# Optimization experiments

Hardware: AMD Instinct MI355X
Metric: run time of the kernel (lower is better)

## Reference

```python
import jax, jax.numpy as jnp
import numpy as np

SMOOTH = 1e-3
EPS = 1e-12


def setup_inputs() -> dict:
    key = jax.random.key(0)
    k1, k2, k3 = jax.random.split(key, 3)
    pred = jax.random.normal(k1, (1, 16, 384, 384), dtype=jnp.float32)
    labels = jax.random.randint(k2, (1, 16, 384, 384), 0, 2, dtype=jnp.int32)
    # stand-in for create_table_neighbour_code_to_surface_area((1,1,1)): 256-entry LUT
    area = jax.random.uniform(k3, (256,), dtype=jnp.float32) * 2.0
    return {"pred": pred, "labels": labels, "area": area}


def _corners(x2):
    # x2: (B, 2, Y+2, X+2) zero-padded slice pair -> (B, 8, (Y+1)*(X+1))
    # corner index k = dz*4 + dy*2 + dx, matching torch unfold(kernel=(2,2), padding=1)
    B, _, Yp, Xp = x2.shape
    Y, X = Yp - 1, Xp - 1
    cs = [x2[:, dz, dy:dy + Y, dx:dx + X]
          for dz in (0, 1) for dy in (0, 1) for dx in (0, 1)]
    return jnp.stack(cs, axis=1).reshape(B, 8, Y * X)


def _surface_dice(pred_sig, labels, area, smooth):
    B, Z, Y, X = pred_sig.shape
    # bases[i, k] = bit k of code i  (== [c=='1' for c in f'{i:08b}'[::-1]])
    bits = jnp.arange(8, dtype=jnp.int32)
    bases = ((jnp.arange(256, dtype=jnp.int32)[:, None] >> bits[None, :]) & 1).astype(jnp.float32)  # (256,8)
    n_bits = bases.sum(1)  # (256,) popcount

    # blank zero slices on both z ends + the unfold's zero padding in y/x
    Pp = jnp.pad(pred_sig, ((0, 0), (1, 1), (1, 1), (1, 1)))
    Lp = jnp.pad(labels.astype(jnp.int32), ((0, 0), (1, 1), (1, 1), (1, 1)))

    def pair(carry, i):
        num, den, vol = carry
        pz = jax.lax.dynamic_slice(Pp, (0, i, 0, 0), (B, 2, Y + 2, X + 2))
        lz = jax.lax.dynamic_slice(Lp, (0, i, 0, 0), (B, 2, Y + 2, X + 2))
        pc = _corners(pz)                      # (B, 8, Np) float
        lc = _corners(lz)                      # (B, 8, Np) int32
        byte = jnp.left_shift(lc, bits[None, :, None]).sum(axis=1)  # (B, Np) label corner code

        # basis_weights = 1 - mean_k (pc_k - bases_ik)^2, expanded so the
        # (B,256,8,Np) broadcast is never materialized
        sp2 = jnp.sum(pc * pc, axis=1)                       # (B, Np)
        cross = jnp.einsum('bkn,ik->bin', pc, bases)         # (B, 256, Np)
        bw = 1.0 - (sp2[:, None, :] + n_bits[None, :, None] - 2.0 * cross) / 8.0

        pred_byte = jnp.argmax(bw, axis=1)                   # (B, Np)
        pred_area = area[pred_byte]                          # (B, Np)
        label_area = area[byte]                              # (B, Np)
        pw = jnp.take_along_axis(bw, byte[:, None, :], axis=1)[:, 0]  # (B, Np)

        # binary_cross_entropy(unfolded_pred, unfolded_labels) per element
        lf = lc.astype(jnp.float32)
        logp = jnp.log(jnp.maximum(pc, EPS))
        log1mp = jnp.log(jnp.maximum(1.0 - pc, EPS))
        bce = -(lf * logp + (1.0 - lf) * log1mp)             # (B, 8, Np)
        interior = (byte == 0) | (byte == 255)               # (B, Np)
        v = jnp.where(interior[:, None, :], bce, 0.0).mean((1, 2))

        inter = jnp.sum(pw * label_area, axis=1)
        return (num + 2.0 * inter,
                den + label_area.sum(1) + pred_area.sum(1),
                vol + v), None

    init = (jnp.zeros((B,), jnp.float32), jnp.zeros((B,), jnp.float32), jnp.zeros((B,), jnp.float32))
    (num, den, vol), _ = jax.lax.scan(pair, init, jnp.arange(Z + 1))
    dice = 1.0 - (num + smooth) / (den + smooth)
    return dice.mean() + vol.mean()


def reference(pred, labels, area):
    return _surface_dice(jax.nn.sigmoid(pred), labels, area, SMOOTH)
```

## Files before the change

kernel.cpp:

```cpp
#include <hip/hip_runtime.h>
#include <math.h>

constexpr int ZN = 16, YN = 384, XN = 384;
constexpr int NZ = 17, NY = 385, NX = 385;
constexpr int NP = NY * NX;
constexpr int NROWS = NZ * NY;
constexpr int BLOCKS = 1637;

__global__ __launch_bounds__(256) void sd_main(
        const float* __restrict__ pred,
        const int*   __restrict__ labels,
        const float* __restrict__ area,
        float*       __restrict__ partial)
{
    __shared__ float s_area[256];
    {
        const int t = threadIdx.x;
        const int own = t >> 4, prv = t & 15;
        int code = 0;
#pragma unroll
        for (int r = 0; r < 4; ++r)
            code |= (((prv >> r) & 1) << (2 * r)) | (((own >> r) & 1) << (2 * r + 1));
        s_area[t] = area[code];
    }
    __syncthreads();

    const int lane = threadIdx.x & 63;
    const int wid  = blockIdx.x * 4 + (threadIdx.x >> 6);

    float num = 0.f, den = 0.f, vol = 0.f;

    if (wid < NROWS) {
        const int z = wid / NY;
        const int y = wid - z * NY;

        bool rv[4]; int base[4];
#pragma unroll
        for (int r = 0; r < 4; ++r) {
            const int zz = z - 1 + (r >> 1);
            const int yy = y - 1 + (r & 1);
            rv[r]   = ((unsigned)zz < (unsigned)ZN) & ((unsigned)yy < (unsigned)YN);
            base[r] = (zz * YN + yy) * XN;
        }

        float cs[4] = {0.f, 0.f, 0.f, 0.f};
        int   cb = 0;

        auto do_node = [&](const float s[4], int LP, const float ps[4], int PLP) {
            const int idxL = ((LP & 15) << 4) | (PLP & 15);
            const int idxP = (LP & 0xF0) | (PLP >> 4);
            const float la = s_area[idxL];
            const float pa = s_area[idxP];
            float u[8];
            float sq = 0.f;
#pragma unroll
            for (int r = 0; r < 4; ++r) {
                const float u0 = ((PLP >> r) & 1) ? ps[r] : 1.f - ps[r];
                const float u1 = ((LP  >> r) & 1) ? s[r]  : 1.f - s[r];
                u[2 * r] = u0; u[2 * r + 1] = u1;
                const float d0 = 1.f - u0, d1 = 1.f - u1;
                sq += d0 * d0 + d1 * d1;
            }
            const float pw = 1.f - sq * 0.125f;
            num += 2.f * pw * la;
            den += la + pa;
            if (idxL == 0 || idxL == 255) {
                float b = 0.f;
#pragma unroll
                for (int k = 0; k < 8; ++k)
                    b += __logf(fmaxf(u[k], 1e-12f));
                vol -= b;
            }
        };

        for (int chunk = 0; chunk < 6; ++chunk) {
            const int x = chunk * 64 + lane;
            float s[4]; int LP = 0;
#pragma unroll
            for (int r = 0; r < 4; ++r) {
                if (rv[r]) {
                    const float p = pred[base[r] + x];
                    const int   l = labels[base[r] + x];
                    s[r] = __fdividef(1.f, 1.f + __expf(-p));
                    LP  |= (l << r) | ((int)(p > 0.f) << (r + 4));
                } else {
                    s[r] = 0.f;
                }
            }
            float ps[4]; int PLP;
#pragma unroll
            for (int r = 0; r < 4; ++r) ps[r] = __shfl_up(s[r], 1);
            PLP = __shfl_up(LP, 1);
            if (lane == 0) {
#pragma unroll
                for (int r = 0; r < 4; ++r) ps[r] = cs[r];
                PLP = cb;
            }
            do_node(s, LP, ps, PLP);
#pragma unroll
            for (int r = 0; r < 4; ++r) cs[r] = __shfl(s[r], 63);
            cb = __shfl(LP, 63);
        }
        if (lane == 0) {
            const float zs[4] = {0.f, 0.f, 0.f, 0.f};
            do_node(zs, 0, cs, cb);
        }
    }

#pragma unroll
    for (int off = 32; off > 0; off >>= 1) {
        num += __shfl_down(num, off);
        den += __shfl_down(den, off);
        vol += __shfl_down(vol, off);
    }
    __shared__ float sn[4], sd_[4], sv[4];
    const int w = threadIdx.x >> 6;
    if (lane == 0) { sn[w] = num; sd_[w] = den; sv[w] = vol; }
    __syncthreads();
    if (threadIdx.x == 0) {
        partial[blockIdx.x]              = sn[0] + sn[1] + sn[2] + sn[3];
        partial[BLOCKS + blockIdx.x]     = sd_[0] + sd_[1] + sd_[2] + sd_[3];
        partial[2 * BLOCKS + blockIdx.x] = sv[0] + sv[1] + sv[2] + sv[3];
    }
}

__global__ __launch_bounds__(256) void sd_final(
        const float* __restrict__ partial, float* __restrict__ out)
{
    double n = 0.0, d = 0.0, v = 0.0;
    for (int b = threadIdx.x; b < BLOCKS; b += 256) {
        n += (double)partial[b];
        d += (double)partial[BLOCKS + b];
        v += (double)partial[2 * BLOCKS + b];
    }
#pragma unroll
    for (int off = 32; off > 0; off >>= 1) {
        n += __shfl_down(n, off);
        d += __shfl_down(d, off);
        v += __shfl_down(v, off);
    }
    __shared__ double sn[4], sd_[4], sv[4];
    const int lane = threadIdx.x & 63, w = threadIdx.x >> 6;
    if (lane == 0) { sn[w] = n; sd_[w] = d; sv[w] = v; }
    __syncthreads();
    if (threadIdx.x == 0) {
        const double num = sn[0] + sn[1] + sn[2] + sn[3];
        const double den = sd_[0] + sd_[1] + sd_[2] + sd_[3];
        const double vol = (sv[0] + sv[1] + sv[2] + sv[3]) / (8.0 * (double)NP);
        const double dice = 1.0 - (num + 1e-3) / (den + 1e-3);
        out[0] = (float)(dice + vol);
    }
}

extern "C" void kernel_launch(void* const* d_in, const int* in_sizes, int n_in,
                              void* d_out, int out_size, void* d_ws, size_t ws_size,
                              hipStream_t stream)
{
    const float* pred   = (const float*)d_in[0];
    const int*   labels = (const int*)d_in[1];
    const float* area   = (const float*)d_in[2];
    float* out     = (float*)d_out;
    float* partial = (float*)d_ws;

    sd_main<<<BLOCKS, 256, 0, stream>>>(pred, labels, area, partial);
    sd_final<<<1, 256, 0, stream>>>(partial, out);
}
```

Before: 89.07 us.

## Process three x-nodes per lane and fuse final reduction via last-block counter

Each lane now handles three consecutive x positions per chunk, which cuts the loop to two iterations and amortizes the shuffles across three nodes. The squared-distance term is precomputed per column pair (q) and reused by adjacent nodes, so it is no longer recomputed from the corner values each time. The separate finalize kernel is replaced by an atomic counter, where the last block to finish reduces the partials, at the cost of a memset launch and a threadfence. The strided per-lane loads (stride 3) may coalesce less well than the previous contiguous per-lane access.

Result: slower. 122.5 us (+37.6%).

```diff
diff --git a/kernel.cpp b/kernel.cpp
--- a/kernel.cpp
+++ b/kernel.cpp
@@ -5,13 +5,15 @@
 constexpr int NZ = 17, NY = 385, NX = 385;
 constexpr int NP = NY * NX;
 constexpr int NROWS = NZ * NY;
-constexpr int BLOCKS = 1637;
+constexpr int BLOCKS = (NROWS + 3) / 4;
 
 __global__ __launch_bounds__(256) void sd_main(
         const float* __restrict__ pred,
         const int*   __restrict__ labels,
         const float* __restrict__ area,
-        float*       __restrict__ partial)
+        int*         __restrict__ counter,
+        float*       __restrict__ partial,
+        float*       __restrict__ out)
 {
     __shared__ float s_area[256];
     {
@@ -43,67 +45,78 @@
             base[r] = (zz * YN + yy) * XN;
         }
 
-        float cs[4] = {0.f, 0.f, 0.f, 0.f};
-        int   cb = 0;
-
-        auto do_node = [&](const float s[4], int LP, const float ps[4], int PLP) {
-            const int idxL = ((LP & 15) << 4) | (PLP & 15);
-            const int idxP = (LP & 0xF0) | (PLP >> 4);
+        auto node = [&](const float* sp, float qp, int bp,
+                        const float* so, float qo, int bo) {
+            const int idxL = ((bo & 15) << 4) | (bp & 15);
+            const int idxP = (bo & 0xF0) | (bp >> 4);
             const float la = s_area[idxL];
             const float pa = s_area[idxP];
-            float u[8];
-            float sq = 0.f;
-#pragma unroll
-            for (int r = 0; r < 4; ++r) {
-                const float u0 = ((PLP >> r) & 1) ? ps[r] : 1.f - ps[r];
-                const float u1 = ((LP  >> r) & 1) ? s[r]  : 1.f - s[r];
-                u[2 * r] = u0; u[2 * r + 1] = u1;
-                const float d0 = 1.f - u0, d1 = 1.f - u1;
-                sq += d0 * d0 + d1 * d1;
-            }
-            const float pw = 1.f - sq * 0.125f;
-            num += 2.f * pw * la;
+            const float pw = 1.f - (qp + qo) * 0.125f;
+            num = fmaf(2.f * la, pw, num);
             den += la + pa;
             if (idxL == 0 || idxL == 255) {
+                const bool one = (idxL == 255);
                 float b = 0.f;
 #pragma unroll
-                for (int k = 0; k < 8; ++k)
-                    b += __logf(fmaxf(u[k], 1e-12f));
+                for (int r = 0; r < 4; ++r) {
+                    const float up = one ? sp[r] : 1.f - sp[r];
+                    const float uo = one ? so[r] : 1.f - so[r];
+                    b += __logf(fmaxf(up, 1e-12f)) + __logf(fmaxf(uo, 1e-12f));
+                }
                 vol -= b;
             }
         };
 
-        for (int chunk = 0; chunk < 6; ++chunk) {
-            const int x = chunk * 64 + lane;
-            float s[4]; int LP = 0;
+        float cs[4] = {0.f, 0.f, 0.f, 0.f};
+        float cq = 0.f; int cbc = 0;
+
+        for (int c = 0; c < 2; ++c) {
+            const int xb = c * 192 + lane * 3;
+            float s[3][4];
+            float q[3]  = {0.f, 0.f, 0.f};
+            int   cb[3] = {0, 0, 0};
 #pragma unroll
             for (int r = 0; r < 4; ++r) {
                 if (rv[r]) {
-                    const float p = pred[base[r] + x];
-                    const int   l = labels[base[r] + x];
-                    s[r] = __fdividef(1.f, 1.f + __expf(-p));
-                    LP  |= (l << r) | ((int)(p > 0.f) << (r + 4));
+                    const float* pp = pred + base[r] + xb;
+                    const int*   lp = labels + base[r] + xb;
+                    float p[3]; int l[3];
+#pragma unroll
+                    for (int j = 0; j < 3; ++j) { p[j] = pp[j]; l[j] = lp[j]; }
+#pragma unroll
+                    for (int j = 0; j < 3; ++j) {
+                        const float sv = __fdividef(1.f, 1.f + __expf(-p[j]));
+                        s[j][r] = sv;
+                        const float d = sv - (float)l[j];
+                        q[j] = fmaf(d, d, q[j]);
+                        cb[j] |= (l[j] << r) | ((int)(p[j] > 0.f) << (r + 4));
+                    }
                 } else {
-                    s[r] = 0.f;
+#pragma unroll
+                    for (int j = 0; j < 3; ++j) s[j][r] = 0.f;
                 }
             }
-            float ps[4]; int PLP;
+            float ps[4]; float pq; int pb;
 #pragma unroll
-            for (int r = 0; r < 4; ++r) ps[r] = __shfl_up(s[r], 1);
-            PLP = __shfl_up(LP, 1);
+            for (int r = 0; r < 4; ++r) ps[r] = __shfl_up(s[2][r], 1);
+            pq = __shfl_up(q[2], 1);
+            pb = __shfl_up(cb[2], 1);
             if (lane == 0) {
 #pragma unroll
                 for (int r = 0; r < 4; ++r) ps[r] = cs[r];
-                PLP = cb;
+                pq = cq; pb = cbc;
             }
-            do_node(s, LP, ps, PLP);
+            node(ps,   pq,   pb,    s[0], q[0], cb[0]);
+            node(s[0], q[0], cb[0], s[1], q[1], cb[1]);
+            node(s[1], q[1], cb[1], s[2], q[2], cb[2]);
 #pragma unroll
-            for (int r = 0; r < 4; ++r) cs[r] = __shfl(s[r], 63);
-            cb = __shfl(LP, 63);
+            for (int r = 0; r < 4; ++r) cs[r] = __shfl(s[2][r], 63);
+            cq  = __shfl(q[2], 63);
+            cbc = __shfl(cb[2], 63);
         }
         if (lane == 0) {
             const float zs[4] = {0.f, 0.f, 0.f, 0.f};
-            do_node(zs, 0, cs, cb);
+            node(cs, cq, cbc, zs, 0.f, 0);
         }
     }
 
@@ -117,38 +130,41 @@
     const int w = threadIdx.x >> 6;
     if (lane == 0) { sn[w] = num; sd_[w] = den; sv[w] = vol; }
     __syncthreads();
+    __shared__ bool amLast;
     if (threadIdx.x == 0) {
         partial[blockIdx.x]              = sn[0] + sn[1] + sn[2] + sn[3];
         partial[BLOCKS + blockIdx.x]     = sd_[0] + sd_[1] + sd_[2] + sd_[3];
         partial[2 * BLOCKS + blockIdx.x] = sv[0] + sv[1] + sv[2] + sv[3];
+        __threadfence();
+        amLast = (atomicAdd(counter, 1) == BLOCKS - 1);
     }
-}
+    __syncthreads();
 
-__global__ __launch_bounds__(256) void sd_final(
-        const float* __restrict__ partial, float* __restrict__ out)
-{
-    double n = 0.0, d = 0.0, v = 0.0;
-    for (int b = threadIdx.x; b < BLOCKS; b += 256) {
-        n += (double)partial[b];
-        d += (double)partial[BLOCKS + b];
-        v += (double)partial[2 * BLOCKS + b];
-    }
+    if (amLast) {
+        __threadfence();
+        const volatile float* vp = (const volatile float*)partial;
+        double n = 0.0, d = 0.0, v = 0.0;
+        for (int b = threadIdx.x; b < BLOCKS; b += 256) {
+            n += (double)vp[b];
+            d += (double)vp[BLOCKS + b];
+            v += (double)vp[2 * BLOCKS + b];
+        }
 #pragma unroll
-    for (int off = 32; off > 0; off >>= 1) {
-        n += __shfl_down(n, off);
-        d += __shfl_down(d, off);
-        v += __shfl_down(v, off);
-    }
-    __shared__ double sn[4], sd_[4], sv[4];
-    const int lane = threadIdx.x & 63, w = threadIdx.x >> 6;
-    if (lane == 0) { sn[w] = n; sd_[w] = d; sv[w] = v; }
-    __syncthreads();
-    if (threadIdx.x == 0) {
-        const double num = sn[0] + sn[1] + sn[2] + sn[3];
-        const double den = sd_[0] + sd_[1] + sd_[2] + sd_[3];
-        const double vol = (sv[0] + sv[1] + sv[2] + sv[3]) / (8.0 * (double)NP);
-        const double dice = 1.0 - (num + 1e-3) / (den + 1e-3);
-        out[0] = (float)(dice + vol);
+        for (int off = 32; off > 0; off >>= 1) {
+            n += __shfl_down(n, off);
+            d += __shfl_down(d, off);
+            v += __shfl_down(v, off);
+        }
+        __shared__ double dn[4], dd[4], dv[4];
+        if (lane == 0) { dn[w] = n; dd[w] = d; dv[w] = v; }
+        __syncthreads();
+        if (threadIdx.x == 0) {
+            const double nn = dn[0] + dn[1] + dn[2] + dn[3];
+            const double dd_ = dd[0] + dd[1] + dd[2] + dd[3];
+            const double vv = (dv[0] + dv[1] + dv[2] + dv[3]) / (8.0 * (double)NP);
+            const double dice = 1.0 - (nn + 1e-3) / (dd_ + 1e-3);
+            out[0] = (float)(dice + vv);
+        }
     }
 }
 
@@ -160,8 +176,9 @@
     const int*   labels = (const int*)d_in[1];
     const float* area   = (const float*)d_in[2];
     float* out     = (float*)d_out;
-    float* partial = (float*)d_ws;
+    int*   counter = (int*)d_ws;
+    float* partial = (float*)((char*)d_ws + 16);
 
-    sd_main<<<BLOCKS, 256, 0, stream>>>(pred, labels, area, partial);
-    sd_final<<<1, 256, 0, stream>>>(partial, out);
+    hipMemsetAsync(counter, 0, 16, stream);
+    sd_main<<<BLOCKS, 256, 0, stream>>>(pred, labels, area, counter, partial, out);
 }
```

## Give each lane six contiguous columns with vector loads and per-column squared error

Applied to the files above, without the earlier changes.

Each lane now handles six adjacent x columns, loaded as float2/int2 vectors, instead of striding over six 64-wide chunks. Adjacent corner pairs are resolved in registers, so only one cross-lane shuffle set is needed per row instead of per chunk. The per-column squared distance to the label is precomputed once and reused by both neighbouring nodes, and the log terms are recomputed only on interior nodes. The cost is higher register pressure and uncoalesced 8-byte strided loads across lanes, with a stride of 24 bytes.

New measurement: 86.70 us. 2.7% less time.

```diff
diff --git a/kernel.cpp b/kernel.cpp
--- a/kernel.cpp
+++ b/kernel.cpp
@@ -5,7 +5,10 @@
 constexpr int NZ = 17, NY = 385, NX = 385;
 constexpr int NP = NY * NX;
 constexpr int NROWS = NZ * NY;
-constexpr int BLOCKS = 1637;
+constexpr int BLOCKS = (NROWS + 3) / 4;
+
+typedef float F2 __attribute__((ext_vector_type(2)));
+typedef int   I2 __attribute__((ext_vector_type(2)));
 
 __global__ __launch_bounds__(256) void sd_main(
         const float* __restrict__ pred,
@@ -34,76 +37,76 @@
         const int z = wid / NY;
         const int y = wid - z * NY;
 
-        bool rv[4]; int base[4];
+        float s[6][4];
+        float q[6]  = {0.f, 0.f, 0.f, 0.f, 0.f, 0.f};
+        int   cb[6] = {0, 0, 0, 0, 0, 0};
+        const int xb = 6 * lane;
+
 #pragma unroll
         for (int r = 0; r < 4; ++r) {
             const int zz = z - 1 + (r >> 1);
             const int yy = y - 1 + (r & 1);
-            rv[r]   = ((unsigned)zz < (unsigned)ZN) & ((unsigned)yy < (unsigned)YN);
-            base[r] = (zz * YN + yy) * XN;
+            const bool rv = ((unsigned)zz < (unsigned)ZN) & ((unsigned)yy < (unsigned)YN);
+            if (rv) {
+                const int base = (zz * YN + yy) * XN + xb;
+                const F2* pp = (const F2*)(pred + base);
+                const I2* lp = (const I2*)(labels + base);
+                const F2 pa_ = pp[0], pb_ = pp[1], pc_ = pp[2];
+                const I2 la_ = lp[0], lb_ = lp[1], lc_ = lp[2];
+                const float p[6] = {pa_.x, pa_.y, pb_.x, pb_.y, pc_.x, pc_.y};
+                const int   l[6] = {la_.x, la_.y, lb_.x, lb_.y, lc_.x, lc_.y};
+#pragma unroll
+                for (int j = 0; j < 6; ++j) {
+                    const float sv = __fdividef(1.f, 1.f + __expf(-p[j]));
+                    s[j][r] = sv;
+                    const float d = sv - (float)l[j];
+                    q[j] = fmaf(d, d, q[j]);
+                    cb[j] |= (l[j] << r) | ((int)(p[j] > 0.f) << (r + 4));
+                }
+            } else {
+#pragma unroll
+                for (int j = 0; j < 6; ++j) s[j][r] = 0.f;
+            }
         }
 
-        float cs[4] = {0.f, 0.f, 0.f, 0.f};
-        int   cb = 0;
-
-        auto do_node = [&](const float s[4], int LP, const float ps[4], int PLP) {
-            const int idxL = ((LP & 15) << 4) | (PLP & 15);
-            const int idxP = (LP & 0xF0) | (PLP >> 4);
+        auto node = [&](const float* sp, float qp, int bp,
+                        const float* so, float qo, int bo) {
+            const int idxL = ((bo & 15) << 4) | (bp & 15);
+            const int idxP = (bo & 0xF0) | (bp >> 4);
             const float la = s_area[idxL];
             const float pa = s_area[idxP];
-            float u[8];
-            float sq = 0.f;
-#pragma unroll
-            for (int r = 0; r < 4; ++r) {
-                const float u0 = ((PLP >> r) & 1) ? ps[r] : 1.f - ps[r];
-                const float u1 = ((LP  >> r) & 1) ? s[r]  : 1.f - s[r];
-                u[2 * r] = u0; u[2 * r + 1] = u1;
-                const float d0 = 1.f - u0, d1 = 1.f - u1;
-                sq += d0 * d0 + d1 * d1;
-            }
-            const float pw = 1.f - sq * 0.125f;
-            num += 2.f * pw * la;
+            const float pw = 1.f - (qp + qo) * 0.125f;
+            num = fmaf(2.f * la, pw, num);
             den += la + pa;
             if (idxL == 0 || idxL == 255) {
+                const bool one = (idxL == 255);
                 float b = 0.f;
 #pragma unroll
-                for (int k = 0; k < 8; ++k)
-                    b += __logf(fmaxf(u[k], 1e-12f));
+                for (int r = 0; r < 4; ++r) {
+                    const float up = one ? sp[r] : 1.f - sp[r];
+                    const float uo = one ? so[r] : 1.f - so[r];
+                    b += __logf(fmaxf(up, 1e-12f)) + __logf(fmaxf(uo, 1e-12f));
+                }
                 vol -= b;
             }
         };
 
-        for (int chunk = 0; chunk < 6; ++chunk) {
-            const int x = chunk * 64 + lane;
-            float s[4]; int LP = 0;
+        float ps[4]; float pq; int pb;
 #pragma unroll
-            for (int r = 0; r < 4; ++r) {
-                if (rv[r]) {
-                    const float p = pred[base[r] + x];
-                    const int   l = labels[base[r] + x];
-                    s[r] = __fdividef(1.f, 1.f + __expf(-p));
-                    LP  |= (l << r) | ((int)(p > 0.f) << (r + 4));
-                } else {
-                    s[r] = 0.f;
-                }
-            }
-            float ps[4]; int PLP;
-#pragma unroll
-            for (int r = 0; r < 4; ++r) ps[r] = __shfl_up(s[r], 1);
-            PLP = __shfl_up(LP, 1);
-            if (lane == 0) {
-#pragma unroll
-                for (int r = 0; r < 4; ++r) ps[r] = cs[r];
-                PLP = cb;
-            }
-            do_node(s, LP, ps, PLP);
-#pragma unroll
-            for (int r = 0; r < 4; ++r) cs[r] = __shfl(s[r], 63);
-            cb = __shfl(LP, 63);
-        }
-        if (lane == 0) {
+        for (int r = 0; r < 4; ++r) ps[r] = __shfl_up(s[5][r], 1);
+        pq = __shfl_up(q[5], 1);
+        pb = __shfl_up(cb[5], 1);
+        if (lane == 0) { ps[0] = ps[1] = ps[2] = ps[3] = 0.f; pq = 0.f; pb = 0; }
+
+        node(ps,   pq,   pb,    s[0], q[0], cb[0]);
+        node(s[0], q[0], cb[0], s[1], q[1], cb[1]);
+        node(s[1], q[1], cb[1], s[2], q[2], cb[2]);
+        node(s[2], q[2], cb[2], s[3], q[3], cb[3]);
+        node(s[3], q[3], cb[3], s[4], q[4], cb[4]);
+        node(s[4], q[4], cb[4], s[5], q[5], cb[5]);
+        if (lane == 63) {
             const float zs[4] = {0.f, 0.f, 0.f, 0.f};
-            do_node(zs, 0, cs, cb);
+            node(s[5], q[5], cb[5], zs, 0.f, 0);
         }
     }
 
```

## Sweep waves along z with register carry of column data to reuse loads

Applied to the files above, without the earlier changes.

Each wave now owns one 64-column chunk of a y-row pair and walks along z, split into two halves. The previous z slice's sigmoid values, squared deviations and label bits stay in registers, so each voxel is loaded and passed through the sigmoid about twice instead of four times. The squared-error term is also precomputed per column as (s-l)^2, which simplifies the per-node math. In exchange the grid has fewer, longer waves with serial z dependence, and lane 0 does extra scalar edge loads.

After: 90.47 us. About the same (+1.6%).

```diff
diff --git a/kernel.cpp b/kernel.cpp
--- a/kernel.cpp
+++ b/kernel.cpp
@@ -4,8 +4,14 @@
 constexpr int ZN = 16, YN = 384, XN = 384;
 constexpr int NZ = 17, NY = 385, NX = 385;
 constexpr int NP = NY * NX;
-constexpr int NROWS = NZ * NY;
-constexpr int BLOCKS = 1637;
+constexpr int NWAVES = NY * 12;
+constexpr int BLOCKS = NWAVES / 4;
+
+struct Col { float s0, s1, q; int b; };
+
+__device__ __forceinline__ float sigm(float p) {
+    return __fdividef(1.f, 1.f + __expf(-p));
+}
 
 __global__ __launch_bounds__(256) void sd_main(
         const float* __restrict__ pred,
@@ -27,84 +33,106 @@
 
     const int lane = threadIdx.x & 63;
     const int wid  = blockIdx.x * 4 + (threadIdx.x >> 6);
+    const int czh  = wid / NY;
+    const int y    = wid - czh * NY;
+    const int c    = czh >> 1;
+    const int zh   = czh & 1;
 
     float num = 0.f, den = 0.f, vol = 0.f;
 
-    if (wid < NROWS) {
-        const int z = wid / NY;
-        const int y = wid - z * NY;
+    const bool v0 = (y >= 1);
+    const bool v1 = (y <= YN - 1);
+    const int  r0 = (y - 1) * XN;
+    const int  r1 = y * XN;
+    const int  x  = c * 64 + lane;
+    const int  xe = c * 64 - 1;
+    const bool ev = (c > 0);
 
-        bool rv[4]; int base[4];
+    auto pp = [&](int zz, int col, bool cok) -> Col {
+        Col r; r.s0 = 0.f; r.s1 = 0.f; r.q = 0.f; r.b = 0;
+        if (((unsigned)zz < (unsigned)ZN) & cok) {
+            const int sb = zz * (YN * XN) + col;
+            if (v0) {
+                const float p = pred[sb + r0]; const int l = labels[sb + r0];
+                const float s = sigm(p);
+                const float d = s - (float)l;
+                r.s0 = s; r.q = d * d;
+                r.b  = l | ((int)(p > 0.f) << 2);
+            }
+            if (v1) {
+                const float p = pred[sb + r1]; const int l = labels[sb + r1];
+                const float s = sigm(p);
+                const float d = s - (float)l;
+                r.s1 = s; r.q += d * d;
+                r.b |= (l << 1) | ((int)(p > 0.f) << 3);
+            }
+        }
+        return r;
+    };
+
+    auto node = [&](float ps0, float ps1, float ps2, float ps3, float pq, int pL, int pP,
+                    float os0, float os1, float os2, float os3, float oq, int oL, int oP) {
+        const int idxL = (oL << 4) | pL;
+        const int idxP = (oP << 4) | pP;
+        const float la = s_area[idxL];
+        const float pa = s_area[idxP];
+        num = fmaf(2.f * la, 1.f - (pq + oq) * 0.125f, num);
+        den += la + pa;
+        if (idxL == 0 || idxL == 255) {
+            const bool one = (idxL == 255);
+            float b = __logf(fmaxf(one ? ps0 : 1.f - ps0, 1e-12f))
+                    + __logf(fmaxf(one ? ps1 : 1.f - ps1, 1e-12f))
+                    + __logf(fmaxf(one ? ps2 : 1.f - ps2, 1e-12f))
+                    + __logf(fmaxf(one ? ps3 : 1.f - ps3, 1e-12f))
+                    + __logf(fmaxf(one ? os0 : 1.f - os0, 1e-12f))
+                    + __logf(fmaxf(one ? os1 : 1.f - os1, 1e-12f))
+                    + __logf(fmaxf(one ? os2 : 1.f - os2, 1e-12f))
+                    + __logf(fmaxf(one ? os3 : 1.f - os3, 1e-12f));
+            vol -= b;
+        }
+    };
+
+    Col o; o.s0 = 0.f; o.s1 = 0.f; o.q = 0.f; o.b = 0;
+    float qs0 = 0.f, qs1 = 0.f, pqo = 0.f; int pbo = 0;
+
+    if (zh) {
+        o = pp(8, x, true);
+        Col oe; oe.s0 = oe.s1 = oe.q = 0.f; oe.b = 0;
+        if (lane == 0) oe = pp(8, xe, ev);
+        qs0 = __shfl_up(o.s0, 1); qs1 = __shfl_up(o.s1, 1);
+        pqo = __shfl_up(o.q, 1);  pbo = __shfl_up(o.b, 1);
+        if (lane == 0) { qs0 = oe.s0; qs1 = oe.s1; pqo = oe.q; pbo = oe.b; }
+    }
+
+    auto body = [&](int z) {
+        Col n = pp(z, x, true);
+        Col ne; ne.s0 = ne.s1 = ne.q = 0.f; ne.b = 0;
+        if (lane == 0) ne = pp(z, xe, ev);
+        float pn0 = __shfl_up(n.s0, 1), pn1 = __shfl_up(n.s1, 1), pqn = __shfl_up(n.q, 1);
+        int   pbn = __shfl_up(n.b, 1);
+        if (lane == 0) { pn0 = ne.s0; pn1 = ne.s1; pqn = ne.q; pbn = ne.b; }
+
+        const int oL = (o.b & 3) | ((n.b & 3) << 2);
+        const int oP = ((o.b >> 2) & 3) | (((n.b >> 2) & 3) << 2);
+        const int pL = (pbo & 3) | ((pbn & 3) << 2);
+        const int pP = ((pbo >> 2) & 3) | (((pbn >> 2) & 3) << 2);
+
+        node(qs0, qs1, pn0, pn1, pqo + pqn, pL, pP,
+             o.s0, o.s1, n.s0, n.s1, o.q + n.q, oL, oP);
+
+        if (c == 5 && lane == 63) {
+            node(o.s0, o.s1, n.s0, n.s1, o.q + n.q, oL, oP,
+                 0.f, 0.f, 0.f, 0.f, 0.f, 0, 0);
+        }
+        o = n; qs0 = pn0; qs1 = pn1; pqo = pqn; pbo = pbn;
+    };
+
+    if (zh == 0) {
 #pragma unroll
-        for (int r = 0; r < 4; ++r) {
-            const int zz = z - 1 + (r >> 1);
-            const int yy = y - 1 + (r & 1);
-            rv[r]   = ((unsigned)zz < (unsigned)ZN) & ((unsigned)yy < (unsigned)YN);
-            base[r] = (zz * YN + yy) * XN;
-        }
-
-        float cs[4] = {0.f, 0.f, 0.f, 0.f};
-        int   cb = 0;
-
-        auto do_node = [&](const float s[4], int LP, const float ps[4], int PLP) {
-            const int idxL = ((LP & 15) << 4) | (PLP & 15);
-            const int idxP = (LP & 0xF0) | (PLP >> 4);
-            const float la = s_area[idxL];
-            const float pa = s_area[idxP];
-            float u[8];
-            float sq = 0.f;
+        for (int z = 0; z < 9; ++z) body(z);
+    } else {
 #pragma unroll
-            for (int r = 0; r < 4; ++r) {
-                const float u0 = ((PLP >> r) & 1) ? ps[r] : 1.f - ps[r];
-                const float u1 = ((LP  >> r) & 1) ? s[r]  : 1.f - s[r];
-                u[2 * r] = u0; u[2 * r + 1] = u1;
-                const float d0 = 1.f - u0, d1 = 1.f - u1;
-                sq += d0 * d0 + d1 * d1;
-            }
-            const float pw = 1.f - sq * 0.125f;
-            num += 2.f * pw * la;
-            den += la + pa;
-            if (idxL == 0 || idxL == 255) {
-                float b = 0.f;
-#pragma unroll
-                for (int k = 0; k < 8; ++k)
-                    b += __logf(fmaxf(u[k], 1e-12f));
-                vol -= b;
-            }
-        };
-
-        for (int chunk = 0; chunk < 6; ++chunk) {
-            const int x = chunk * 64 + lane;
-            float s[4]; int LP = 0;
-#pragma unroll
-            for (int r = 0; r < 4; ++r) {
-                if (rv[r]) {
-                    const float p = pred[base[r] + x];
-                    const int   l = labels[base[r] + x];
-                    s[r] = __fdividef(1.f, 1.f + __expf(-p));
-                    LP  |= (l << r) | ((int)(p > 0.f) << (r + 4));
-                } else {
-                    s[r] = 0.f;
-                }
-            }
-            float ps[4]; int PLP;
-#pragma unroll
-            for (int r = 0; r < 4; ++r) ps[r] = __shfl_up(s[r], 1);
-            PLP = __shfl_up(LP, 1);
-            if (lane == 0) {
-#pragma unroll
-                for (int r = 0; r < 4; ++r) ps[r] = cs[r];
-                PLP = cb;
-            }
-            do_node(s, LP, ps, PLP);
-#pragma unroll
-            for (int r = 0; r < 4; ++r) cs[r] = __shfl(s[r], 63);
-            cb = __shfl(LP, 63);
-        }
-        if (lane == 0) {
-            const float zs[4] = {0.f, 0.f, 0.f, 0.f};
-            do_node(zs, 0, cs, cb);
-        }
+        for (int z = 9; z < 17; ++z) body(z);
     }
 
 #pragma unroll
```
